# Kernel optimization log

Hardware: AMD Instinct MI355X
Metric: run time of the kernel (lower is better)

## Reference

```python
import jax, jax.numpy as jnp
import numpy as np

B, T, C, HS = 8, 2048, 1024, 64
NEG_INF = float('-inf')


def setup_inputs() -> dict:
    key = jax.random.key(0)
    kx, kk, kq, kv = jax.random.split(key, 4)
    scale = 1.0 / np.sqrt(C)
    return {
        'x': jax.random.normal(kx, (B, T, C), dtype=jnp.float32),
        'Wk': jax.random.normal(kk, (C, HS), dtype=jnp.float32) * scale,
        'Wq': jax.random.normal(kq, (C, HS), dtype=jnp.float32) * scale,
        'Wv': jax.random.normal(kv, (C, HS), dtype=jnp.float32) * scale,
    }


def reference(x, Wk, Wq, Wv):
    b, t, c = x.shape
    k = x @ Wk          # [b, t, hs]
    q = x @ Wq          # [b, t, hs]
    v = x @ Wv          # [b, t, hs]
    # NOTE: original scales by c**-0.5 where c = input embed dim (not head_size)
    wei = jnp.einsum('bth,bsh->bts', q, k) * (c ** -0.5)  # [b, t(query), t(key)]
    # causal mask: position (i, j) valid iff j <= i
    causal = jnp.tril(jnp.ones((t, t), dtype=bool))
    wei = jnp.where(causal, wei, NEG_INF)
    # NOTE: original applies softmax over dim=1 (the QUERY axis) — reproduced faithfully
    wei = jax.nn.softmax(wei, axis=1)
    # dropout p=0.0 / eval mode -> identity
    return jnp.einsum('bts,bsh->bth', wei, v)  # [b, t, hs]
```

## Files before the change

kernel.cpp:

```cpp
#include <hip/hip_runtime.h>
#include <hip/hip_bf16.h>

namespace {

typedef unsigned short u16;
typedef __attribute__((ext_vector_type(8))) short bf16x8;
typedef __attribute__((ext_vector_type(4))) float f32x4;

constexpr int kB = 8, kT = 2048, kC = 1024, kH = 64;
constexpr float kScale = 0.03125f;

constexpr size_t kWtOff = 0;
constexpr size_t kQbOff = kWtOff + 3 * 64 * 1024;
constexpr size_t kKbOff = kQbOff + (size_t)16384 * 64;
constexpr size_t kVtOff = kKbOff + (size_t)16384 * 64;
constexpr size_t kLOff  = kVtOff + (size_t)16384 * 64;
constexpr size_t kPartOff = kLOff + (size_t)16384 * 2;

__device__ __forceinline__ u16 f2bu(float f) {
  __hip_bfloat16 h = __float2bfloat16(f);
  return *reinterpret_cast<u16*>(&h);
}
__device__ __forceinline__ f32x4 mfma16(bf16x8 a, bf16x8 b, f32x4 c) {
  return __builtin_amdgcn_mfma_f32_16x16x32_bf16(a, b, c, 0, 0, 0);
}

__global__ __launch_bounds__(256) void zero_l_kernel(float* __restrict__ l) {
  l[blockIdx.x * 256 + threadIdx.x] = 0.f;
}

__global__ __launch_bounds__(256) void wt_kernel(
    const float* __restrict__ Wk, const float* __restrict__ Wq,
    const float* __restrict__ Wv, u16* __restrict__ Wt) {
  __shared__ float wsm[64 * 65];
  const int c0 = blockIdx.x * 64;
  const int mat = blockIdx.y;
  const float* W = (mat == 0) ? Wk : (mat == 1) ? Wq : Wv;
  const int tid = threadIdx.x;
#pragma unroll
  for (int ii = 0; ii < 4; ++ii) {
    const int p = tid + 256 * ii;
    const int row = p >> 4, col4 = p & 15;
    const float4 wv = *reinterpret_cast<const float4*>(&W[(size_t)(c0 + row) * 64 + col4 * 4]);
    wsm[row * 65 + col4 * 4 + 0] = wv.x;
    wsm[row * 65 + col4 * 4 + 1] = wv.y;
    wsm[row * 65 + col4 * 4 + 2] = wv.z;
    wsm[row * 65 + col4 * 4 + 3] = wv.w;
  }
  __syncthreads();
  const int h = tid & 63, seg = tid >> 6;
#pragma unroll
  for (int i = 0; i < 16; ++i) {
    const int c = seg * 16 + i;
    Wt[((size_t)mat * 64 + h) * 1024 + c0 + c] = f2bu(wsm[c * 65 + h]);
  }
}

__global__ __launch_bounds__(256) void qkv_kernel(
    const float* __restrict__ x, const u16* __restrict__ Wt,
    u16* __restrict__ qb, u16* __restrict__ kb, u16* __restrict__ vt) {
  __shared__ u16 wl[192 * 128];
  __shared__ u16 xl[32 * 128];
  const int tid = threadIdx.x;
  const int lane = tid & 63, w = tid >> 6;
  const int l15 = lane & 15, l4 = lane >> 4;
  const int m0 = blockIdx.x * 32;

  f32x4 acc[2][3];
#pragma unroll
  for (int mi = 0; mi < 2; ++mi)
#pragma unroll
    for (int ni = 0; ni < 3; ++ni) acc[mi][ni] = f32x4{0.f, 0.f, 0.f, 0.f};

  for (int p = 0; p < 8; ++p) {
    const int k0 = p * 128;
    __syncthreads();
#pragma unroll
    for (int i = 0; i < 12; ++i) {
      const int q = tid + 256 * i;
      const int row = q >> 4, c8 = (q & 15) * 8;
      const uint4 wv = *reinterpret_cast<const uint4*>(&Wt[(size_t)row * 1024 + k0 + c8]);
      *reinterpret_cast<uint4*>(&wl[(row * 128 + c8) ^ ((row & 7) << 3)]) = wv;
    }
#pragma unroll
    for (int i = 0; i < 4; ++i) {
      const int q = tid + 256 * i;
      const int row = q >> 5, c4 = (q & 31) * 4;
      const float4 xv = *reinterpret_cast<const float4*>(&x[(size_t)(m0 + row) * kC + k0 + c4]);
      uint2 pk;
      pk.x = (unsigned)f2bu(xv.x) | ((unsigned)f2bu(xv.y) << 16);
      pk.y = (unsigned)f2bu(xv.z) | ((unsigned)f2bu(xv.w) << 16);
      *reinterpret_cast<uint2*>(&xl[(row * 128 + c4) ^ ((row & 7) << 3)]) = pk;
    }
    __syncthreads();
#pragma unroll
    for (int ks = 0; ks < 4; ++ks) {
      const int kk = ks * 32 + 8 * l4;
      bf16x8 a[2];
#pragma unroll
      for (int mi = 0; mi < 2; ++mi) {
        const int row = 16 * mi + l15;
        a[mi] = *reinterpret_cast<const bf16x8*>(&xl[(row * 128 + kk) ^ ((row & 7) << 3)]);
      }
#pragma unroll
      for (int ni = 0; ni < 3; ++ni) {
        const int row = 48 * w + 16 * ni + l15;
        const bf16x8 bfr =
            *reinterpret_cast<const bf16x8*>(&wl[(row * 128 + kk) ^ ((row & 7) << 3)]);
#pragma unroll
        for (int mi = 0; mi < 2; ++mi) acc[mi][ni] = mfma16(a[mi], bfr, acc[mi][ni]);
      }
    }
  }
#pragma unroll
  for (int ni = 0; ni < 3; ++ni) {
    const int ncol = 48 * w + 16 * ni + l15;
    const int mat = ncol >> 6, h = ncol & 63;
#pragma unroll
    for (int mi = 0; mi < 2; ++mi) {
#pragma unroll
      for (int r = 0; r < 4; ++r) {
        const int m = m0 + 16 * mi + 4 * l4 + r;
        const u16 val = f2bu(acc[mi][ni][r]);
        if (mat == 0) kb[(size_t)m * 64 + h] = val;
        else if (mat == 1) qb[(size_t)m * 64 + h] = val;
        else vt[((size_t)((m >> 11) * 64 + h)) * 2048 + (m & 2047)] = val;
      }
    }
  }
}

__global__ __launch_bounds__(256) void colsum_kernel(
    const u16* __restrict__ qb, const u16* __restrict__ kb, float* __restrict__ lG) {
  const int bid = blockIdx.x;
  const int b = bid & 7;
  const int rr = bid >> 3;
  const int s0 = (rr & 31) * 64;
  const int tc = (rr >> 5) * 512;
  if (tc + 511 < s0) return;
  const int tid = threadIdx.x;
  const int lane = tid & 63, w = tid >> 6;
  const int l15 = lane & 15, l4 = lane >> 4;

  bf16x8 ka[4][2];
#pragma unroll
  for (int i = 0; i < 4; ++i) {
    const u16* kp = kb + (size_t)(b * kT + s0 + 16 * i + l15) * 64 + 8 * l4;
    ka[i][0] = *reinterpret_cast<const bf16x8*>(kp);
    ka[i][1] = *reinterpret_cast<const bf16x8*>(kp + 32);
  }
  f32x4 cs[4];
#pragma unroll
  for (int i = 0; i < 4; ++i) cs[i] = f32x4{0.f, 0.f, 0.f, 0.f};

  const int d0 = s0 - tc - 128 * w;
  const int jstart = (d0 > 0) ? (d0 >> 4) : 0;
  const u16* qbase = qb + (size_t)(b * kT + tc + 128 * w + l15) * 64 + 8 * l4;
  bf16x8 qf0, qf1;
  if (jstart < 8) {
    qf0 = *reinterpret_cast<const bf16x8*>(qbase + (size_t)jstart * 1024);
    qf1 = *reinterpret_cast<const bf16x8*>(qbase + (size_t)jstart * 1024 + 32);
  }
  for (int j = jstart; j < 8; ++j) {
    bf16x8 qn0, qn1;
    if (j < 7) {
      qn0 = *reinterpret_cast<const bf16x8*>(qbase + (size_t)(j + 1) * 1024);
      qn1 = *reinterpret_cast<const bf16x8*>(qbase + (size_t)(j + 1) * 1024 + 32);
    }
    const int t = tc + 128 * w + 16 * j + l15;
#pragma unroll
    for (int i = 0; i < 4; ++i) {
      f32x4 d = f32x4{0.f, 0.f, 0.f, 0.f};
      d = mfma16(ka[i][0], qf0, d);
      d = mfma16(ka[i][1], qf1, d);
#pragma unroll
      for (int r = 0; r < 4; ++r) {
        const int s = s0 + 16 * i + 4 * l4 + r;
        if (t >= s) cs[i][r] += __expf(d[r] * kScale);
      }
    }
    qf0 = qn0; qf1 = qn1;
  }
#pragma unroll
  for (int i = 0; i < 4; ++i) {
#pragma unroll
    for (int r = 0; r < 4; ++r) {
      float v = cs[i][r];
      v += __shfl_xor(v, 1, 64);
      v += __shfl_xor(v, 2, 64);
      v += __shfl_xor(v, 4, 64);
      v += __shfl_xor(v, 8, 64);
      if (l15 == 0) atomicAdd(&lG[b * kT + s0 + 16 * i + 4 * l4 + r], v);
    }
  }
}

__global__ __launch_bounds__(512, 4) void out_part_kernel(
    const u16* __restrict__ qb, const u16* __restrict__ kb, const u16* __restrict__ vt,
    const float* __restrict__ lG, float* __restrict__ part) {
  __shared__ u16 kl[64 * 64];
  __shared__ u16 vl[64 * 64];
  const int bid = blockIdx.x;
  const int b = bid & 7;
  const int q4 = (bid >> 3) & 3;
  const int tt = bid >> 5;
  const int t0 = tt * 128;
  const int tid = threadIdx.x;
  const int lane = tid & 63, w = tid >> 6;
  const int l15 = lane & 15, l4 = lane >> 4;
  const size_t bT = (size_t)b * kT;
  const int sA = l15 + 32 * (l4 & 1);
  const int sB = sA + 16;
  const bool hi = l4 >= 2;
  const int srow = tid >> 3, sc8 = (tid & 7) * 8;
  const int sidx = (srow * 64 + sc8) ^ ((srow & 7) << 3);

  const int tw = t0 + 16 * w;
  const u16* qp = qb + (bT + tw + l15) * 64 + 8 * l4;
  const bf16x8 qf0 = *reinterpret_cast<const bf16x8*>(qp);
  const bf16x8 qf1 = *reinterpret_cast<const bf16x8*>(qp + 32);

  f32x4 acc[4];
#pragma unroll
  for (int nf = 0; nf < 4; ++nf) acc[nf] = f32x4{0.f, 0.f, 0.f, 0.f};

  const int js0 = q4 * 8;
  const int js1 = min(js0 + 8, 2 * tt + 2);
  for (int js = js0; js < js1; ++js) {
    const int s0 = js * 64;
    __syncthreads();
    *reinterpret_cast<uint4*>(&kl[sidx]) =
        *reinterpret_cast<const uint4*>(&kb[(bT + s0 + srow) * 64 + sc8]);
    *reinterpret_cast<uint4*>(&vl[sidx]) =
        *reinterpret_cast<const uint4*>(&vt[(size_t)(b * 64 + srow) * kT + s0 + sc8]);
    __syncthreads();
    if (tw + 15 < s0) continue;

    float4 lv[4];
#pragma unroll
    for (int jf = 0; jf < 4; ++jf)
      lv[jf] = *reinterpret_cast<const float4*>(&lG[bT + s0 + 16 * jf + 4 * l4]);

    unsigned pk0[4], pk1[4];
    const int t = tw + l15;
    const bool masked = (s0 + 63 > tw);
#pragma unroll
    for (int jf = 0; jf < 4; ++jf) {
      const int krow = 16 * jf + l15;
      const bf16x8 kf0 = *reinterpret_cast<const bf16x8*>(
          &kl[(krow * 64 + 8 * l4) ^ ((krow & 7) << 3)]);
      const bf16x8 kf1 = *reinterpret_cast<const bf16x8*>(
          &kl[(krow * 64 + 32 + 8 * l4) ^ ((krow & 7) << 3)]);
      f32x4 d = f32x4{0.f, 0.f, 0.f, 0.f};
      d = mfma16(kf0, qf0, d);
      d = mfma16(kf1, qf1, d);
      const float rl0 = __builtin_amdgcn_rcpf(lv[jf].x);
      const float rl1 = __builtin_amdgcn_rcpf(lv[jf].y);
      const float rl2 = __builtin_amdgcn_rcpf(lv[jf].z);
      const float rl3 = __builtin_amdgcn_rcpf(lv[jf].w);
      float p[4];
      if (masked) {
        const int sb = s0 + 16 * jf + 4 * l4;
        p[0] = (t >= sb + 0) ? __expf(d[0] * kScale) * rl0 : 0.f;
        p[1] = (t >= sb + 1) ? __expf(d[1] * kScale) * rl1 : 0.f;
        p[2] = (t >= sb + 2) ? __expf(d[2] * kScale) * rl2 : 0.f;
        p[3] = (t >= sb + 3) ? __expf(d[3] * kScale) * rl3 : 0.f;
      } else {
        p[0] = __expf(d[0] * kScale) * rl0;
        p[1] = __expf(d[1] * kScale) * rl1;
        p[2] = __expf(d[2] * kScale) * rl2;
        p[3] = __expf(d[3] * kScale) * rl3;
      }
      pk0[jf] = (unsigned)f2bu(p[0]) | ((unsigned)f2bu(p[1]) << 16);
      pk1[jf] = (unsigned)f2bu(p[2]) | ((unsigned)f2bu(p[3]) << 16);
    }
    {
      const unsigned a0 = __shfl(pk0[0], sA), a1 = __shfl(pk1[0], sA);
      const unsigned a2 = __shfl(pk0[0], sB), a3 = __shfl(pk1[0], sB);
      const unsigned b0 = __shfl(pk0[1], sA), b1 = __shfl(pk1[1], sA);
      const unsigned b2 = __shfl(pk0[1], sB), b3 = __shfl(pk1[1], sB);
      uint4 pw;
      pw.x = hi ? b0 : a0; pw.y = hi ? b1 : a1;
      pw.z = hi ? b2 : a2; pw.w = hi ? b3 : a3;
      const bf16x8 pa = *reinterpret_cast<const bf16x8*>(&pw);
#pragma unroll
      for (int nf = 0; nf < 4; ++nf) {
        const int vrow = 16 * nf + l15;
        const bf16x8 vf = *reinterpret_cast<const bf16x8*>(
            &vl[(vrow * 64 + 8 * l4) ^ ((vrow & 7) << 3)]);
        acc[nf] = mfma16(pa, vf, acc[nf]);
      }
    }
    {
      const unsigned a0 = __shfl(pk0[2], sA), a1 = __shfl(pk1[2], sA);
      const unsigned a2 = __shfl(pk0[2], sB), a3 = __shfl(pk1[2], sB);
      const unsigned b0 = __shfl(pk0[3], sA), b1 = __shfl(pk1[3], sA);
      const unsigned b2 = __shfl(pk0[3], sB), b3 = __shfl(pk1[3], sB);
      uint4 pw;
      pw.x = hi ? b0 : a0; pw.y = hi ? b1 : a1;
      pw.z = hi ? b2 : a2; pw.w = hi ? b3 : a3;
      const bf16x8 pa = *reinterpret_cast<const bf16x8*>(&pw);
#pragma unroll
      for (int nf = 0; nf < 4; ++nf) {
        const int vrow = 16 * nf + l15;
        const bf16x8 vf = *reinterpret_cast<const bf16x8*>(
            &vl[(vrow * 64 + 32 + 8 * l4) ^ ((vrow & 7) << 3)]);
        acc[nf] = mfma16(pa, vf, acc[nf]);
      }
    }
  }
  float* pb = part + (size_t)(q4 * 8 + b) * kT * kH;
#pragma unroll
  for (int nf = 0; nf < 4; ++nf) {
#pragma unroll
    for (int r = 0; r < 4; ++r) {
      pb[(size_t)(tw + 4 * l4 + r) * 64 + 16 * nf + l15] = acc[nf][r];
    }
  }
}

__global__ __launch_bounds__(256) void combine_kernel(
    const float* __restrict__ part, float* __restrict__ out) {
  const size_t i = ((size_t)blockIdx.x * 256 + threadIdx.x) * 4;
  const float4 p0 = *reinterpret_cast<const float4*>(part + i);
  const float4 p1 = *reinterpret_cast<const float4*>(part + 1048576 + i);
  const float4 p2 = *reinterpret_cast<const float4*>(part + 2097152 + i);
  const float4 p3 = *reinterpret_cast<const float4*>(part + 3145728 + i);
  float4 s;
  s.x = p0.x + p1.x + p2.x + p3.x;
  s.y = p0.y + p1.y + p2.y + p3.y;
  s.z = p0.z + p1.z + p2.z + p3.z;
  s.w = p0.w + p1.w + p2.w + p3.w;
  *reinterpret_cast<float4*>(out + i) = s;
}

}

extern "C" void kernel_launch(void* const* d_in, const int* in_sizes, int n_in,
                              void* d_out, int out_size, void* d_ws, size_t ws_size,
                              hipStream_t stream) {
  const float* x = (const float*)d_in[0];
  const float* Wk = (const float*)d_in[1];
  const float* Wq = (const float*)d_in[2];
  const float* Wv = (const float*)d_in[3];
  u16* wsu = (u16*)d_ws;
  u16* Wt = wsu + kWtOff;
  u16* qb = wsu + kQbOff;
  u16* kb = wsu + kKbOff;
  u16* vt = wsu + kVtOff;
  float* lG = (float*)(wsu + kLOff);
  float* part = (float*)(wsu + kPartOff);
  float* out = (float*)d_out;

  zero_l_kernel<<<dim3(kB * kT / 256), dim3(256), 0, stream>>>(lG);
  wt_kernel<<<dim3(16, 3), dim3(256), 0, stream>>>(Wk, Wq, Wv, Wt);
  qkv_kernel<<<dim3(kB * kT / 32), dim3(256), 0, stream>>>(x, Wt, qb, kb, vt);
  colsum_kernel<<<dim3(1024), dim3(256), 0, stream>>>(qb, kb, lG);
  out_part_kernel<<<dim3(512), dim3(512), 0, stream>>>(qb, kb, vt, lG, part);
  combine_kernel<<<dim3(1024), dim3(256), 0, stream>>>(part, out);
}
```

Before: 74.30 us.

## Restructure column-sum pass with LDS-shared Q tiles and deterministic partial sums

Rewrites the softmax-denominator kernel so each 512-thread block stages 64-row Q tiles in swizzled LDS, shared by 8 waves that each hold one 16-row K fragment. Work is split into four query-range partitions. Each partition writes its partial column sums to its own buffer, so atomics are not needed. A small combine kernel sums the four partitions, which removes the zero-initialisation launch. The intent is to cut redundant global Q loads and atomic contention. In exchange it adds barriers per tile, some masked wasted work near the diagonal, and an extra kernel launch.

```diff
diff --git a/kernel.cpp b/kernel.cpp
--- a/kernel.cpp
+++ b/kernel.cpp
@@ -16,6 +16,7 @@
 constexpr size_t kVtOff = kKbOff + (size_t)16384 * 64;
 constexpr size_t kLOff  = kVtOff + (size_t)16384 * 64;
 constexpr size_t kPartOff = kLOff + (size_t)16384 * 2;
+constexpr size_t kLPartOff = kPartOff + (size_t)4 * 1048576 * 2;
 
 __device__ __forceinline__ u16 f2bu(float f) {
   __hip_bfloat16 h = __float2bfloat16(f);
@@ -23,10 +24,6 @@
 }
 __device__ __forceinline__ f32x4 mfma16(bf16x8 a, bf16x8 b, f32x4 c) {
   return __builtin_amdgcn_mfma_f32_16x16x32_bf16(a, b, c, 0, 0, 0);
-}
-
-__global__ __launch_bounds__(256) void zero_l_kernel(float* __restrict__ l) {
-  l[blockIdx.x * 256 + threadIdx.x] = 0.f;
 }
 
 __global__ __launch_bounds__(256) void wt_kernel(
@@ -130,69 +127,82 @@
   }
 }
 
-__global__ __launch_bounds__(256) void colsum_kernel(
-    const u16* __restrict__ qb, const u16* __restrict__ kb, float* __restrict__ lG) {
+__global__ __launch_bounds__(512) void colsum_part_kernel(
+    const u16* __restrict__ qb, const u16* __restrict__ kb, float* __restrict__ lpart) {
+  __shared__ u16 ql[64 * 64];
   const int bid = blockIdx.x;
   const int b = bid & 7;
-  const int rr = bid >> 3;
-  const int s0 = (rr & 31) * 64;
-  const int tc = (rr >> 5) * 512;
-  if (tc + 511 < s0) return;
+  const int q4 = (bid >> 3) & 3;
+  const int ss = bid >> 5;
   const int tid = threadIdx.x;
   const int lane = tid & 63, w = tid >> 6;
   const int l15 = lane & 15, l4 = lane >> 4;
-
-  bf16x8 ka[4][2];
-#pragma unroll
-  for (int i = 0; i < 4; ++i) {
-    const u16* kp = kb + (size_t)(b * kT + s0 + 16 * i + l15) * 64 + 8 * l4;
-    ka[i][0] = *reinterpret_cast<const bf16x8*>(kp);
-    ka[i][1] = *reinterpret_cast<const bf16x8*>(kp + 32);
-  }
-  f32x4 cs[4];
-#pragma unroll
-  for (int i = 0; i < 4; ++i) cs[i] = f32x4{0.f, 0.f, 0.f, 0.f};
-
-  const int d0 = s0 - tc - 128 * w;
-  const int jstart = (d0 > 0) ? (d0 >> 4) : 0;
-  const u16* qbase = qb + (size_t)(b * kT + tc + 128 * w + l15) * 64 + 8 * l4;
-  bf16x8 qf0, qf1;
-  if (jstart < 8) {
-    qf0 = *reinterpret_cast<const bf16x8*>(qbase + (size_t)jstart * 1024);
-    qf1 = *reinterpret_cast<const bf16x8*>(qbase + (size_t)jstart * 1024 + 32);
-  }
-  for (int j = jstart; j < 8; ++j) {
-    bf16x8 qn0, qn1;
-    if (j < 7) {
-      qn0 = *reinterpret_cast<const bf16x8*>(qbase + (size_t)(j + 1) * 1024);
-      qn1 = *reinterpret_cast<const bf16x8*>(qbase + (size_t)(j + 1) * 1024 + 32);
-    }
-    const int t = tc + 128 * w + 16 * j + l15;
-#pragma unroll
-    for (int i = 0; i < 4; ++i) {
+  const size_t bT = (size_t)b * kT;
+  const int srow = tid >> 3, sc8 = (tid & 7) * 8;
+  const int sidx = (srow * 64 + sc8) ^ ((srow & 7) << 3);
+
+  const int sw = ss * 128 + 16 * w;
+  const u16* kp = kb + (bT + sw + l15) * 64 + 8 * l4;
+  const bf16x8 ka0 = *reinterpret_cast<const bf16x8*>(kp);
+  const bf16x8 ka1 = *reinterpret_cast<const bf16x8*>(kp + 32);
+
+  float cs[4] = {0.f, 0.f, 0.f, 0.f};
+
+  const int jt0 = max(q4 * 8, 2 * ss);
+  const int jt1 = q4 * 8 + 8;
+  for (int jt = jt0; jt < jt1; ++jt) {
+    const int t0 = jt * 64;
+    __syncthreads();
+    *reinterpret_cast<uint4*>(&ql[sidx]) =
+        *reinterpret_cast<const uint4*>(&qb[(bT + t0 + srow) * 64 + sc8]);
+    __syncthreads();
+    const bool masked = (t0 < sw + 15);
+#pragma unroll
+    for (int c = 0; c < 4; ++c) {
+      const int tl = 16 * c + l15;
+      const bf16x8 qf0 = *reinterpret_cast<const bf16x8*>(
+          &ql[(tl * 64 + 8 * l4) ^ ((tl & 7) << 3)]);
+      const bf16x8 qf1 = *reinterpret_cast<const bf16x8*>(
+          &ql[(tl * 64 + 32 + 8 * l4) ^ ((tl & 7) << 3)]);
       f32x4 d = f32x4{0.f, 0.f, 0.f, 0.f};
-      d = mfma16(ka[i][0], qf0, d);
-      d = mfma16(ka[i][1], qf1, d);
-#pragma unroll
-      for (int r = 0; r < 4; ++r) {
-        const int s = s0 + 16 * i + 4 * l4 + r;
-        if (t >= s) cs[i][r] += __expf(d[r] * kScale);
-      }
-    }
-    qf0 = qn0; qf1 = qn1;
-  }
-#pragma unroll
-  for (int i = 0; i < 4; ++i) {
-#pragma unroll
-    for (int r = 0; r < 4; ++r) {
-      float v = cs[i][r];
-      v += __shfl_xor(v, 1, 64);
-      v += __shfl_xor(v, 2, 64);
-      v += __shfl_xor(v, 4, 64);
-      v += __shfl_xor(v, 8, 64);
-      if (l15 == 0) atomicAdd(&lG[b * kT + s0 + 16 * i + 4 * l4 + r], v);
-    }
-  }
+      d = mfma16(ka0, qf0, d);
+      d = mfma16(ka1, qf1, d);
+      if (masked) {
+        const int t = t0 + 16 * c + l15;
+        const int sb = sw + 4 * l4;
+#pragma unroll
+        for (int r = 0; r < 4; ++r)
+          if (t >= sb + r) cs[r] += __expf(d[r] * kScale);
+      } else {
+#pragma unroll
+        for (int r = 0; r < 4; ++r) cs[r] += __expf(d[r] * kScale);
+      }
+    }
+  }
+#pragma unroll
+  for (int r = 0; r < 4; ++r) {
+    float v = cs[r];
+    v += __shfl_xor(v, 1, 64);
+    v += __shfl_xor(v, 2, 64);
+    v += __shfl_xor(v, 4, 64);
+    v += __shfl_xor(v, 8, 64);
+    if (l15 == 0) lpart[(size_t)q4 * (kB * kT) + bT + sw + 4 * l4 + r] = v;
+  }
+}
+
+__global__ __launch_bounds__(256) void lcombine_kernel(
+    const float* __restrict__ lpart, float* __restrict__ lG) {
+  const size_t i = ((size_t)blockIdx.x * 256 + threadIdx.x) * 4;
+  const float4 p0 = *reinterpret_cast<const float4*>(lpart + i);
+  const float4 p1 = *reinterpret_cast<const float4*>(lpart + 16384 + i);
+  const float4 p2 = *reinterpret_cast<const float4*>(lpart + 32768 + i);
+  const float4 p3 = *reinterpret_cast<const float4*>(lpart + 49152 + i);
+  float4 s;
+  s.x = p0.x + p1.x + p2.x + p3.x;
+  s.y = p0.y + p1.y + p2.y + p3.y;
+  s.z = p0.z + p1.z + p2.z + p3.z;
+  s.w = p0.w + p1.w + p2.w + p3.w;
+  *reinterpret_cast<float4*>(lG + i) = s;
 }
 
 __global__ __launch_bounds__(512, 4) void out_part_kernel(
@@ -350,12 +360,13 @@
   u16* vt = wsu + kVtOff;
   float* lG = (float*)(wsu + kLOff);
   float* part = (float*)(wsu + kPartOff);
+  float* lpart = (float*)(wsu + kLPartOff);
   float* out = (float*)d_out;
 
-  zero_l_kernel<<<dim3(kB * kT / 256), dim3(256), 0, stream>>>(lG);
   wt_kernel<<<dim3(16, 3), dim3(256), 0, stream>>>(Wk, Wq, Wv, Wt);
   qkv_kernel<<<dim3(kB * kT / 32), dim3(256), 0, stream>>>(x, Wt, qb, kb, vt);
-  colsum_kernel<<<dim3(1024), dim3(256), 0, stream>>>(qb, kb, lG);
+  colsum_part_kernel<<<dim3(512), dim3(512), 0, stream>>>(qb, kb, lpart);
+  lcombine_kernel<<<dim3(16), dim3(256), 0, stream>>>(lpart, lG);
   out_part_kernel<<<dim3(512), dim3(512), 0, stream>>>(qb, kb, vt, lG, part);
   combine_kernel<<<dim3(1024), dim3(256), 0, stream>>>(part, out);
 }
```

Result: faster. 66.57 us, median of 2 (-10.4%).
